# Kernel optimization log

Hardware: AMD Instinct MI355X
Metric: run time of the kernel (lower is better)

The kernel has to match this reference:

```python
import jax, jax.numpy as jnp
import numpy as np

H = 2048       # hidden_size
NH = 16        # num_attention_heads
NKV = 4        # num_key_value_heads
HD = H // NH   # head_dim = 128
INTER = 8192   # intermediate_size
L = 2048       # packed sequence length
EPS = 1e-6


def rmsnorm(x, w, eps=EPS):
    var = jnp.mean(x * x, axis=-1, keepdims=True)
    return x * jax.lax.rsqrt(var + eps) * w


def setup_inputs() -> dict:
    key = jax.random.key(0)
    ks = jax.random.split(key, 9)
    s = 0.02
    return {
        "hidden_states": jax.random.normal(ks[0], (1, L, H), jnp.float32),
        "cu_seqlens_q": jnp.array([0, 512, 1280, 2048], jnp.int32),
        "ln1_w": jnp.ones((H,), jnp.float32),
        "ln2_w": jnp.ones((H,), jnp.float32),
        "q_w": jax.random.normal(ks[1], (NH * HD, H), jnp.float32) * s,
        "k_w": jax.random.normal(ks[2], (NKV * HD, H), jnp.float32) * s,
        "v_w": jax.random.normal(ks[3], (NKV * HD, H), jnp.float32) * s,
        "o_w": jax.random.normal(ks[4], (H, NH * HD), jnp.float32) * s,
        "gate_w": jax.random.normal(ks[5], (INTER, H), jnp.float32) * s,
        "up_w": jax.random.normal(ks[6], (INTER, H), jnp.float32) * s,
        "down_w": jax.random.normal(ks[7], (H, INTER), jnp.float32) * s,
    }


def _segment_mask(cu, q_len):
    # segment id of each position: repeat_interleave of arange over lengths
    pos = jnp.arange(q_len)
    seg = jnp.searchsorted(cu[1:], pos, side="right")  # [L]
    mask = seg[:, None] == seg[None, :]
    mask = mask & (pos[None, :] <= pos[:, None])  # causal, q_len == k_len
    return mask  # [L, L] bool


def _forward(hidden_states, cu_seqlens_q, ln1_w, ln2_w, q_w, k_w, v_w, o_w,
             gate_w, up_w, down_w):
    b, q_len, _ = hidden_states.shape
    residual = hidden_states
    normed = rmsnorm(hidden_states, ln1_w)

    # project_kv
    key_states = (normed @ k_w.T).reshape(b, q_len, NKV, HD)
    value_states = (normed @ v_w.T).reshape(b, q_len, NKV, HD)

    q = (normed @ q_w.T).reshape(b, q_len, NH, HD)
    rep = NH // NKV
    k = jnp.repeat(key_states, rep, axis=2)   # repeat_interleave over heads
    v = jnp.repeat(value_states, rep, axis=2)

    scores = jnp.einsum("bqhd,bkhd->bhqk", q, k) / np.sqrt(HD)
    mask = _segment_mask(cu_seqlens_q, q_len)
    scores = jnp.where(mask[None, None, :, :], scores,
                       jnp.finfo(scores.dtype).min)
    probs = jax.nn.softmax(scores.astype(jnp.float32), axis=-1).astype(q.dtype)
    attn = jnp.einsum("bhqk,bkhd->bqhd", probs, v).reshape(b, q_len, NH * HD)
    mixed = attn @ o_w.T

    hidden = residual + mixed
    residual = hidden
    normed2 = rmsnorm(hidden, ln2_w)
    mlp = (jax.nn.silu(normed2 @ gate_w.T) * (normed2 @ up_w.T)) @ down_w.T
    hidden = residual + mlp
    return hidden, key_states, value_states


def reference(hidden_states, cu_seqlens_q, ln1_w, ln2_w, q_w, k_w, v_w, o_w,
              gate_w, up_w, down_w):
    return _forward(hidden_states, cu_seqlens_q, ln1_w, ln2_w, q_w, k_w, v_w,
                    o_w, gate_w, up_w, down_w)
```

## Files before the change

kernel.cpp:

```cpp
#include <hip/hip_runtime.h>
#include <stdint.h>

typedef __bf16 bf16;
typedef __bf16 bf16x8 __attribute__((ext_vector_type(8)));
typedef __bf16 bf16x4v __attribute__((ext_vector_type(4)));
typedef float f32x4 __attribute__((ext_vector_type(4)));

#define L_SEQ 2048
#define H_DIM 2048
#define KV_DIM 512
#define QKV_LD 3072
#define INTER_DIM 8192

__device__ __forceinline__ void load_lds16(const void* g, void* l) {
  __builtin_amdgcn_global_load_lds(
      (const __attribute__((address_space(1))) void*)g,
      (__attribute__((address_space(3))) void*)l, 16, 0, 0);
}

__global__ __launch_bounds__(256)
void cvt_all(const float* __restrict__ q, const float* __restrict__ k,
             const float* __restrict__ v, const float* __restrict__ o,
             const float* __restrict__ g, const float* __restrict__ u,
             const float* __restrict__ dn, bf16* __restrict__ WB) {
  const int b = blockIdx.x;
  const float* s;
  size_t doff;
  int lb;
  if (b < 2048)       { s = q;  doff = 0;        lb = b; }
  else if (b < 2560)  { s = k;  doff = 4194304;  lb = b - 2048; }
  else if (b < 3072)  { s = v;  doff = 5242880;  lb = b - 2560; }
  else if (b < 5120)  { s = o;  doff = 6291456;  lb = b - 3072; }
  else if (b < 13312) { s = g;  doff = 10485760; lb = b - 5120; }
  else if (b < 21504) { s = u;  doff = 27262976; lb = b - 13312; }
  else                { s = dn; doff = 44040192; lb = b - 21504; }
  const size_t i = (size_t)lb * 2048 + threadIdx.x * 8;
  float4 a = *(const float4*)(s + i);
  float4 c = *(const float4*)(s + i + 4);
  bf16x8 ov;
  ov[0] = (bf16)a.x; ov[1] = (bf16)a.y; ov[2] = (bf16)a.z; ov[3] = (bf16)a.w;
  ov[4] = (bf16)c.x; ov[5] = (bf16)c.y; ov[6] = (bf16)c.z; ov[7] = (bf16)c.w;
  *(bf16x8*)(WB + doff + i) = ov;
}

__global__ __launch_bounds__(256)
void rmsnorm_bf16(const float* __restrict__ x, const float* __restrict__ w,
                  bf16* __restrict__ out) {
  const int row = blockIdx.x;
  const int t = threadIdx.x;
  const float* xr = x + (size_t)row * H_DIM + t * 8;
  float4 a = *(const float4*)xr;
  float4 b = *(const float4*)(xr + 4);
  float ss = a.x * a.x + a.y * a.y + a.z * a.z + a.w * a.w +
             b.x * b.x + b.y * b.y + b.z * b.z + b.w * b.w;
#pragma unroll
  for (int off = 1; off < 64; off <<= 1) ss += __shfl_xor(ss, off, 64);
  __shared__ float red[4];
  if ((t & 63) == 0) red[t >> 6] = ss;
  __syncthreads();
  ss = red[0] + red[1] + red[2] + red[3];
  const float rs = rsqrtf(ss * (1.0f / H_DIM) + 1e-6f);
  float4 w1 = *(const float4*)(w + t * 8);
  float4 w2 = *(const float4*)(w + t * 8 + 4);
  bf16x8 o;
  o[0] = (bf16)(a.x * rs * w1.x);
  o[1] = (bf16)(a.y * rs * w1.y);
  o[2] = (bf16)(a.z * rs * w1.z);
  o[3] = (bf16)(a.w * rs * w1.w);
  o[4] = (bf16)(b.x * rs * w2.x);
  o[5] = (bf16)(b.y * rs * w2.y);
  o[6] = (bf16)(b.z * rs * w2.z);
  o[7] = (bf16)(b.w * rs * w2.w);
  *(bf16x8*)(out + (size_t)row * H_DIM + t * 8) = o;
}

__global__ __launch_bounds__(256)
void add_rmsnorm(const float* __restrict__ p0, const float* __restrict__ p1,
                 const float* __restrict__ res, const float* __restrict__ w,
                 float* __restrict__ hidden, bf16* __restrict__ normed) {
  const int row = blockIdx.x;
  const int t = threadIdx.x;
  const size_t base = (size_t)row * H_DIM + t * 8;
  float4 a0 = *(const float4*)(p0 + base);
  float4 a1 = *(const float4*)(p0 + base + 4);
  float4 b0 = *(const float4*)(p1 + base);
  float4 b1 = *(const float4*)(p1 + base + 4);
  float4 c0 = *(const float4*)(res + base);
  float4 c1 = *(const float4*)(res + base + 4);
  float4 h0, h1;
  h0.x = a0.x + b0.x + c0.x; h0.y = a0.y + b0.y + c0.y;
  h0.z = a0.z + b0.z + c0.z; h0.w = a0.w + b0.w + c0.w;
  h1.x = a1.x + b1.x + c1.x; h1.y = a1.y + b1.y + c1.y;
  h1.z = a1.z + b1.z + c1.z; h1.w = a1.w + b1.w + c1.w;
  *(float4*)(hidden + base) = h0;
  *(float4*)(hidden + base + 4) = h1;
  float ss = h0.x * h0.x + h0.y * h0.y + h0.z * h0.z + h0.w * h0.w +
             h1.x * h1.x + h1.y * h1.y + h1.z * h1.z + h1.w * h1.w;
#pragma unroll
  for (int off = 1; off < 64; off <<= 1) ss += __shfl_xor(ss, off, 64);
  __shared__ float red[4];
  if ((t & 63) == 0) red[t >> 6] = ss;
  __syncthreads();
  ss = red[0] + red[1] + red[2] + red[3];
  const float rs = rsqrtf(ss * (1.0f / H_DIM) + 1e-6f);
  float4 w1 = *(const float4*)(w + t * 8);
  float4 w2 = *(const float4*)(w + t * 8 + 4);
  bf16x8 o;
  o[0] = (bf16)(h0.x * rs * w1.x);
  o[1] = (bf16)(h0.y * rs * w1.y);
  o[2] = (bf16)(h0.z * rs * w1.z);
  o[3] = (bf16)(h0.w * rs * w1.w);
  o[4] = (bf16)(h1.x * rs * w2.x);
  o[5] = (bf16)(h1.y * rs * w2.y);
  o[6] = (bf16)(h1.z * rs * w2.z);
  o[7] = (bf16)(h1.w * rs * w2.w);
  *(bf16x8*)(normed + (size_t)row * H_DIM + t * 8) = o;
}

__global__ __launch_bounds__(256)
void reduce_add4(const float* __restrict__ p, size_t zs,
                 const float* __restrict__ res, float* __restrict__ out) {
  const size_t i = ((size_t)blockIdx.x * 256 + threadIdx.x) * 4;
  float4 a = *(const float4*)(p + i);
  float4 b = *(const float4*)(p + zs + i);
  float4 c = *(const float4*)(p + 2 * zs + i);
  float4 d = *(const float4*)(p + 3 * zs + i);
  float4 r = *(const float4*)(res + i);
  float4 o;
  o.x = a.x + b.x + c.x + d.x + r.x;
  o.y = a.y + b.y + c.y + d.y + r.y;
  o.z = a.z + b.z + c.z + d.z + r.z;
  o.w = a.w + b.w + c.w + d.w + r.w;
  *(float4*)(out + i) = o;
}

__global__ __launch_bounds__(256)
void qkv_combine(const float* __restrict__ p, size_t zs,
                 bf16* __restrict__ qkv, float* __restrict__ outk,
                 float* __restrict__ outv) {
  const size_t i = ((size_t)blockIdx.x * 256 + threadIdx.x) * 4;
  float4 a = *(const float4*)(p + i);
  float4 b = *(const float4*)(p + zs + i);
  float4 s;
  s.x = a.x + b.x; s.y = a.y + b.y; s.z = a.z + b.z; s.w = a.w + b.w;
  bf16x4v o;
  o[0] = (bf16)s.x; o[1] = (bf16)s.y; o[2] = (bf16)s.z; o[3] = (bf16)s.w;
  *(bf16x4v*)(qkv + i) = o;
  const int col = (int)(i % QKV_LD);
  const size_t row = i / QKV_LD;
  if (col >= 2560)      *(float4*)(outv + row * KV_DIM + (col - 2560)) = s;
  else if (col >= 2048) *(float4*)(outk + row * KV_DIM + (col - 2048)) = s;
}


#define WAIT_VM(n) asm volatile("s_waitcnt vmcnt(" #n ")" ::: "memory")

#define ISSUE_TILE(ko, base)                          \
  load_lds16(pa0 + (ko), (base) + dln);               \
  load_lds16(pa1 + (ko), (base) + 8192 + dln);        \
  load_lds16(pb0 + (ko), (base) + 16384 + dln);       \
  load_lds16(pb1 + (ko), (base) + 24576 + dln);

#define MFMA_Q(mh, nh, bfr)                                                  \
  _Pragma("unroll") for (int mi = 0; mi < 4; ++mi)                           \
      _Pragma("unroll") for (int ni = 0; ni < 2; ++ni)                       \
          acc[mh][nh][mi][ni] = __builtin_amdgcn_mfma_f32_16x16x32_bf16(     \
              af[mi], bfr[ni], acc[mh][nh][mi][ni], 0, 0, 0);

__global__ __launch_bounds__(512, 2)
void gemm32_bt(const bf16* __restrict__ A, int lda,
               const bf16* __restrict__ B, int ldb, int kpb,
               float* __restrict__ outf, int ldof, size_t zstride) {
  __shared__ __align__(16) char smb[98304];
  const int t = threadIdx.x;
  const int lane = t & 63;
  const int l15 = lane & 15, l4 = lane >> 4;
  const int wid = t >> 6;
  const int wr = wid >> 2, wc = wid & 3;

  const int gn = gridDim.x;
  const int bid = blockIdx.y * gn + blockIdx.x;
  int mb, nb;
  if ((gn & 7) == 0) {
    const int j = bid & 7, local = bid >> 3, npx = gn >> 3;
    nb = j * npx + local % npx;
    mb = local / npx;
  } else {
    nb = bid % gn;
    mb = bid / gn;
  }
  const int m0 = mb * 256, n0 = nb * 256;
  const int kbeg = blockIdx.z * kpb;
  const int NT = kpb >> 5;

  int aoff[4], boff[2];
#pragma unroll
  for (int mi = 0; mi < 4; ++mi) {
    const int rA = wr * 64 + mi * 16 + l15;
    aoff[mi] = rA * 64 + ((l4 ^ ((rA >> 1) & 3)) << 4);
  }
#pragma unroll
  for (int ni = 0; ni < 2; ++ni) {
    const int rB = wc * 32 + ni * 16 + l15;
    boff[ni] = rB * 64 + ((l4 ^ ((rB >> 1) & 3)) << 4);
  }

  const int r = t >> 2;
  const int gsw = (((t & 3) ^ ((r >> 1) & 3)) << 3);
  const bf16* pa0 = A + (size_t)(m0 + r) * lda + kbeg + gsw;
  const bf16* pa1 = A + (size_t)(m0 + 128 + r) * lda + kbeg + gsw;
  const bf16* pb0 = B + (size_t)(n0 + r) * ldb + kbeg + gsw;
  const bf16* pb1 = B + (size_t)(n0 + 128 + r) * ldb + kbeg + gsw;
  const int dln = t * 16;

  ISSUE_TILE(0, smb);
  if (NT > 1) { ISSUE_TILE(32, smb + 32768); }

  const f32x4 zero = {0.f, 0.f, 0.f, 0.f};
  f32x4 acc[2][2][4][2];
#pragma unroll
  for (int mh = 0; mh < 2; ++mh)
#pragma unroll
    for (int nh = 0; nh < 2; ++nh)
#pragma unroll
      for (int mi = 0; mi < 4; ++mi)
#pragma unroll
        for (int ni = 0; ni < 2; ++ni) acc[mh][nh][mi][ni] = zero;

  int br = 0, bw = 2;
#pragma unroll 1
  for (int tt = 0; tt < NT; ++tt) {
    if (tt + 1 < NT) { WAIT_VM(4); } else { WAIT_VM(0); }
    __builtin_amdgcn_s_barrier();
    if (tt + 2 < NT) {
      char* dst = smb + bw * 32768;
      const int ko = (tt + 2) * 32;
      ISSUE_TILE(ko, dst);
    }
    const char* bb = smb + br * 32768;
    const char* cA0 = bb;
    const char* cA1 = bb + 8192;
    const char* cB0 = bb + 16384;
    const char* cB1 = bb + 24576;

    bf16x8 af[4], b0f[2], b1f[2];
#pragma unroll
    for (int mi = 0; mi < 4; ++mi)
      af[mi] = *(const bf16x8*)(cA0 + aoff[mi]);
#pragma unroll
    for (int ni = 0; ni < 2; ++ni) b0f[ni] = *(const bf16x8*)(cB0 + boff[ni]);
#pragma unroll
    for (int ni = 0; ni < 2; ++ni) b1f[ni] = *(const bf16x8*)(cB1 + boff[ni]);
    MFMA_Q(0, 0, b0f);
    MFMA_Q(0, 1, b1f);
#pragma unroll
    for (int mi = 0; mi < 4; ++mi)
      af[mi] = *(const bf16x8*)(cA1 + aoff[mi]);
    MFMA_Q(1, 0, b0f);
    MFMA_Q(1, 1, b1f);

    br = (br == 2) ? 0 : br + 1;
    bw = (bw == 2) ? 0 : bw + 1;
  }

  float* outz = outf + zstride * blockIdx.z;
#pragma unroll
  for (int mh = 0; mh < 2; ++mh)
#pragma unroll
    for (int nh = 0; nh < 2; ++nh)
#pragma unroll
      for (int mi = 0; mi < 4; ++mi)
#pragma unroll
        for (int ni = 0; ni < 2; ++ni) {
          const int row0 = m0 + mh * 128 + wr * 64 + mi * 16 + l4 * 4;
          const int col = n0 + nh * 128 + wc * 32 + ni * 16 + l15;
#pragma unroll
          for (int rr2 = 0; rr2 < 4; ++rr2)
            outz[(size_t)(row0 + rr2) * ldof + col] = acc[mh][nh][mi][ni][rr2];
        }
}

__global__ __launch_bounds__(512, 2)
void gemm32_glu(const bf16* __restrict__ A, const bf16* __restrict__ Bg,
                const bf16* __restrict__ Bu, bf16* __restrict__ out) {
  __shared__ __align__(16) char smb[98304];
  const int t = threadIdx.x;
  const int lane = t & 63;
  const int l15 = lane & 15, l4 = lane >> 4;
  const int wid = t >> 6;
  const int wr = wid >> 2, wc = wid & 3;

  const int gn = gridDim.x;
  const int bid = blockIdx.y * gn + blockIdx.x;
  const int j = bid & 7, local = bid >> 3, npx = gn >> 3;
  const int nb = j * npx + local % npx;
  const int mb = local / npx;
  const int m0 = mb * 256, n0 = nb * 128;
  const int NT = H_DIM / 32;

  int aoff[4], boff[2];
#pragma unroll
  for (int mi = 0; mi < 4; ++mi) {
    const int rA = wr * 64 + mi * 16 + l15;
    aoff[mi] = rA * 64 + ((l4 ^ ((rA >> 1) & 3)) << 4);
  }
#pragma unroll
  for (int ni = 0; ni < 2; ++ni) {
    const int rB = wc * 32 + ni * 16 + l15;
    boff[ni] = rB * 64 + ((l4 ^ ((rB >> 1) & 3)) << 4);
  }

  const int r = t >> 2;
  const int gsw = (((t & 3) ^ ((r >> 1) & 3)) << 3);
  const bf16* pa0 = A + (size_t)(m0 + r) * H_DIM + gsw;
  const bf16* pa1 = A + (size_t)(m0 + 128 + r) * H_DIM + gsw;
  const bf16* pb0 = Bg + (size_t)(n0 + r) * H_DIM + gsw;
  const bf16* pb1 = Bu + (size_t)(n0 + r) * H_DIM + gsw;
  const int dln = t * 16;

  ISSUE_TILE(0, smb);
  ISSUE_TILE(32, smb + 32768);

  const f32x4 zero = {0.f, 0.f, 0.f, 0.f};
  f32x4 acc[2][2][4][2];
#pragma unroll
  for (int mh = 0; mh < 2; ++mh)
#pragma unroll
    for (int nh = 0; nh < 2; ++nh)
#pragma unroll
      for (int mi = 0; mi < 4; ++mi)
#pragma unroll
        for (int ni = 0; ni < 2; ++ni) acc[mh][nh][mi][ni] = zero;

  int br = 0, bw = 2;
#pragma unroll 1
  for (int tt = 0; tt < NT; ++tt) {
    if (tt + 1 < NT) { WAIT_VM(4); } else { WAIT_VM(0); }
    __builtin_amdgcn_s_barrier();
    if (tt + 2 < NT) {
      char* dst = smb + bw * 32768;
      const int ko = (tt + 2) * 32;
      ISSUE_TILE(ko, dst);
    }
    const char* bb = smb + br * 32768;
    const char* cA0 = bb;
    const char* cA1 = bb + 8192;
    const char* cB0 = bb + 16384;
    const char* cB1 = bb + 24576;

    bf16x8 af[4], b0f[2], b1f[2];
#pragma unroll
    for (int mi = 0; mi < 4; ++mi)
      af[mi] = *(const bf16x8*)(cA0 + aoff[mi]);
#pragma unroll
    for (int ni = 0; ni < 2; ++ni) b0f[ni] = *(const bf16x8*)(cB0 + boff[ni]);
#pragma unroll
    for (int ni = 0; ni < 2; ++ni) b1f[ni] = *(const bf16x8*)(cB1 + boff[ni]);
    MFMA_Q(0, 0, b0f);
    MFMA_Q(0, 1, b1f);
#pragma unroll
    for (int mi = 0; mi < 4; ++mi)
      af[mi] = *(const bf16x8*)(cA1 + aoff[mi]);
    MFMA_Q(1, 0, b0f);
    MFMA_Q(1, 1, b1f);

    br = (br == 2) ? 0 : br + 1;
    bw = (bw == 2) ? 0 : bw + 1;
  }

#pragma unroll
  for (int mh = 0; mh < 2; ++mh)
#pragma unroll
    for (int mi = 0; mi < 4; ++mi)
#pragma unroll
      for (int ni = 0; ni < 2; ++ni) {
        const int row0 = m0 + mh * 128 + wr * 64 + mi * 16 + l4 * 4;
        const int col = n0 + wc * 32 + ni * 16 + l15;
#pragma unroll
        for (int rr2 = 0; rr2 < 4; ++rr2) {
          const float g = acc[mh][0][mi][ni][rr2];
          const float u = acc[mh][1][mi][ni][rr2];
          const float sg = g / (1.f + __expf(-g));
          out[(size_t)(row0 + rr2) * INTER_DIM + col] = (bf16)(sg * u);
        }
      }
}

__global__ __launch_bounds__(256, 3)
void gemm_bt(const bf16* __restrict__ A, int lda,
             const bf16* __restrict__ B, int ldb, int kpb,
             float* __restrict__ outf, int ldof, size_t zstride) {
  __shared__ bf16 sA[2 * 128 * 32];
  __shared__ bf16 sB[2 * 128 * 32];
  const int t = threadIdx.x;
  const int lane = t & 63;
  const int l15 = lane & 15, l4 = lane >> 4;
  const int wm = ((t >> 6) >> 1) * 64;
  const int wn = ((t >> 6) & 1) * 64;
  const int m0 = blockIdx.y * 128;
  const int n0 = blockIdx.x * 128;
  const int kbeg = blockIdx.z * kpb;
  const int kend = kbeg + kpb;

  const f32x4 zero = {0.f, 0.f, 0.f, 0.f};
  f32x4 acc[4][4];
#pragma unroll
  for (int i = 0; i < 4; ++i)
#pragma unroll
    for (int j = 0; j < 4; ++j) acc[i][j] = zero;

  for (int k0 = kbeg; k0 < kend; k0 += 64) {
#pragma unroll
    for (int i = 0; i < 4; ++i) {
      const int flat = i * 4096 + t * 16;
      const int kc = flat >> 13;
      const int wb = flat & 8191;
      const int r = wb >> 6, ce = (wb & 63) >> 1;
      const int gc = k0 + kc * 32 + ce;
      load_lds16(A + (size_t)(m0 + r) * lda + gc, (char*)sA + flat);
      load_lds16(B + (size_t)(n0 + r) * ldb + gc, (char*)sB + flat);
    }
    __syncthreads();

#pragma unroll
    for (int kc = 0; kc < 2; ++kc) {
      bf16x8 af[4], bfr[4];
#pragma unroll
      for (int mi = 0; mi < 4; ++mi)
        af[mi] = *(const bf16x8*)(&sA[kc * 4096 + (wm + mi * 16 + l15) * 32 +
                                      l4 * 8]);
#pragma unroll
      for (int ni = 0; ni < 4; ++ni)
        bfr[ni] = *(const bf16x8*)(&sB[kc * 4096 + (wn + ni * 16 + l15) * 32 +
                                       l4 * 8]);
#pragma unroll
      for (int mi = 0; mi < 4; ++mi)
#pragma unroll
        for (int ni = 0; ni < 4; ++ni)
          acc[mi][ni] = __builtin_amdgcn_mfma_f32_16x16x32_bf16(
              af[mi], bfr[ni], acc[mi][ni], 0, 0, 0);
    }
    __syncthreads();
  }

#pragma unroll
  for (int mi = 0; mi < 4; ++mi) {
#pragma unroll
    for (int ni = 0; ni < 4; ++ni) {
      const int row0 = m0 + wm + mi * 16 + l4 * 4;
      const int col = n0 + wn + ni * 16 + l15;
#pragma unroll
      for (int r = 0; r < 4; ++r)
        outf[zstride * blockIdx.z + (size_t)(row0 + r) * ldof + col] =
            acc[mi][ni][r];
    }
  }
}

__global__ __launch_bounds__(256, 2)
void attn_fwd(const bf16* __restrict__ qkv, const int* __restrict__ cu,
              bf16* __restrict__ out) {
  const int h = blockIdx.y;
  const int q0 = blockIdx.x * 64;
  const int kvh = h >> 2;
  const int t = threadIdx.x;
  const int lane = t & 63;
  const int w = t >> 6;
  const int l15 = lane & 15, l4 = lane >> 4;

  __shared__ bf16 sK[64 * 136];
  __shared__ bf16 sVt[128 * 72];
  __shared__ bf16 sP[4][16 * 64];

  const int c1 = cu[1], c2 = cu[2];
  const int seg0 = (q0 >= c2) ? c2 : ((q0 >= c1) ? c1 : 0);

  const int qrow = q0 + w * 16 + l15;
  bf16x8 qf[4];
#pragma unroll
  for (int kc = 0; kc < 4; ++kc) {
    bf16x8 v = *(const bf16x8*)(qkv + (size_t)qrow * QKV_LD + h * 128 +
                                kc * 32 + l4 * 8);
#pragma unroll
    for (int j = 0; j < 8; ++j)
      v[j] = (bf16)((float)v[j] * 0.08838834764831845f);
    qf[kc] = v;
  }

  const f32x4 zero = {0.f, 0.f, 0.f, 0.f};
  f32x4 oacc[8];
#pragma unroll
  for (int i = 0; i < 8; ++i) oacc[i] = zero;
  float mi[4] = {-1e30f, -1e30f, -1e30f, -1e30f};
  float li[4] = {0.f, 0.f, 0.f, 0.f};

  for (int k0 = seg0; k0 <= q0; k0 += 64) {
#pragma unroll
    for (int it = 0; it < 4; ++it) {
      const int flat = it * 4096 + t * 16;
      const int r = flat >> 8, db = flat & 255;
      *(bf16x8*)((char*)sK + r * 272 + db) = *(const bf16x8*)(
          (const char*)(qkv + (size_t)(k0 + r) * QKV_LD + 2048 + kvh * 128) +
          db);
      const int chunk = it * 256 + t;
      const int vr = chunk & 63, dc = chunk >> 6;
      bf16x8 vv = *(const bf16x8*)(qkv + (size_t)(k0 + vr) * QKV_LD + 2560 +
                                   kvh * 128 + dc * 8);
#pragma unroll
      for (int j = 0; j < 8; ++j) sVt[(dc * 8 + j) * 72 + vr] = vv[j];
    }
    __syncthreads();

    f32x4 sacc[4];
#pragma unroll
    for (int kg = 0; kg < 4; ++kg) {
      f32x4 a = zero;
#pragma unroll
      for (int kc = 0; kc < 4; ++kc) {
        bf16x8 kf = *(const bf16x8*)((const char*)sK + (kg * 16 + l15) * 272 +
                                     kc * 64 + l4 * 16);
        a = __builtin_amdgcn_mfma_f32_16x16x32_bf16(qf[kc], kf, a, 0, 0, 0);
      }
      sacc[kg] = a;
    }

    if (k0 == q0) {
#pragma unroll
      for (int kg = 0; kg < 4; ++kg) {
        const int kk = kg * 16 + l15;
#pragma unroll
        for (int r = 0; r < 4; ++r) {
          const int qq = w * 16 + l4 * 4 + r;
          if (kk > qq) sacc[kg][r] = -1e30f;
        }
      }
    }

    float mx[4], al[4], rs[4];
#pragma unroll
    for (int r = 0; r < 4; ++r)
      mx[r] = fmaxf(fmaxf(sacc[0][r], sacc[1][r]),
                    fmaxf(sacc[2][r], sacc[3][r]));
#pragma unroll
    for (int off = 1; off < 16; off <<= 1)
#pragma unroll
      for (int r = 0; r < 4; ++r)
        mx[r] = fmaxf(mx[r], __shfl_xor(mx[r], off, 64));
#pragma unroll
    for (int r = 0; r < 4; ++r) {
      const float mn = fmaxf(mi[r], mx[r]);
      al[r] = __expf(mi[r] - mn);
      mi[r] = mn;
      rs[r] = 0.f;
    }
#pragma unroll
    for (int kg = 0; kg < 4; ++kg)
#pragma unroll
      for (int r = 0; r < 4; ++r) {
        const float p = __expf(sacc[kg][r] - mi[r]);
        sacc[kg][r] = p;
        rs[r] += p;
      }
#pragma unroll
    for (int off = 1; off < 16; off <<= 1)
#pragma unroll
      for (int r = 0; r < 4; ++r) rs[r] += __shfl_xor(rs[r], off, 64);
#pragma unroll
    for (int r = 0; r < 4; ++r) li[r] = li[r] * al[r] + rs[r];
#pragma unroll
    for (int dn = 0; dn < 8; ++dn)
#pragma unroll
      for (int r = 0; r < 4; ++r) oacc[dn][r] *= al[r];

#pragma unroll
    for (int kg = 0; kg < 4; ++kg)
#pragma unroll
      for (int r = 0; r < 4; ++r)
        sP[w][(l4 * 4 + r) * 64 + kg * 16 + l15] = (bf16)sacc[kg][r];

    bf16x8 pf[2];
#pragma unroll
    for (int kc2 = 0; kc2 < 2; ++kc2)
      pf[kc2] = *(const bf16x8*)(&sP[w][l15 * 64 + kc2 * 32 + l4 * 8]);
#pragma unroll
    for (int dn = 0; dn < 8; ++dn)
#pragma unroll
      for (int kc2 = 0; kc2 < 2; ++kc2) {
        bf16x8 vf = *(const bf16x8*)(&sVt[(dn * 16 + l15) * 72 + kc2 * 32 +
                                          l4 * 8]);
        oacc[dn] = __builtin_amdgcn_mfma_f32_16x16x32_bf16(pf[kc2], vf,
                                                           oacc[dn], 0, 0, 0);
      }
    __syncthreads();
  }

#pragma unroll
  for (int dn = 0; dn < 8; ++dn)
#pragma unroll
    for (int r = 0; r < 4; ++r) {
      const size_t m = (size_t)(q0 + w * 16 + l4 * 4 + r);
      out[m * H_DIM + h * 128 + dn * 16 + l15] = (bf16)(oacc[dn][r] / li[r]);
    }
}

extern "C" void kernel_launch(void* const* d_in, const int* in_sizes, int n_in,
                              void* d_out, int out_size, void* d_ws,
                              size_t ws_size, hipStream_t stream) {
  (void)in_sizes; (void)n_in; (void)out_size; (void)ws_size;
  const float* hs     = (const float*)d_in[0];
  const int*   cu     = (const int*)d_in[1];
  const float* ln1    = (const float*)d_in[2];
  const float* ln2    = (const float*)d_in[3];
  const float* q_w    = (const float*)d_in[4];
  const float* k_w    = (const float*)d_in[5];
  const float* v_w    = (const float*)d_in[6];
  const float* o_w    = (const float*)d_in[7];
  const float* gate_w = (const float*)d_in[8];
  const float* up_w   = (const float*)d_in[9];
  const float* down_w = (const float*)d_in[10];

  float* out_hidden = (float*)d_out;
  float* out_k = out_hidden + (size_t)L_SEQ * H_DIM;
  float* out_v = out_k + (size_t)L_SEQ * KV_DIM;

  char* ws = (char*)d_ws;
  bf16* WB = (bf16*)ws;
  const size_t wq_off = 0;
  const size_t wo_off = 6291456;
  const size_t wg_off = 10485760;
  const size_t wu_off = 27262976;
  const size_t wd_off = 44040192;

  bf16*  normed1 = (bf16*)(ws + ((size_t)116 << 20));
  bf16*  qkv     = (bf16*)(ws + ((size_t)124 << 20));
  bf16*  attnb   = (bf16*)(ws + ((size_t)136 << 20));
  bf16*  normed2 = (bf16*)(ws + ((size_t)144 << 20));
  bf16*  interb  = (bf16*)(ws + ((size_t)152 << 20));
  float* qpart   = (float*)(ws + ((size_t)136 << 20));
  float* opart   = (float*)(ws + ((size_t)152 << 20));
  float* dpart   = (float*)(ws);

  dim3 blk(256);

  cvt_all<<<29696, blk, 0, stream>>>(q_w, k_w, v_w, o_w, gate_w, up_w, down_w,
                                     WB);

  rmsnorm_bf16<<<L_SEQ, blk, 0, stream>>>(hs, ln1, normed1);

  gemm32_bt<<<dim3(12, 8, 2), dim3(512), 0, stream>>>(
      normed1, H_DIM, WB + wq_off, H_DIM, 1024, qpart, QKV_LD,
      (size_t)L_SEQ * QKV_LD);
  qkv_combine<<<6144, blk, 0, stream>>>(qpart, (size_t)L_SEQ * QKV_LD, qkv,
                                        out_k, out_v);

  attn_fwd<<<dim3(32, 16), blk, 0, stream>>>(qkv, cu, attnb);

  gemm_bt<<<dim3(16, 16, 2), blk, 0, stream>>>(
      attnb, H_DIM, WB + wo_off, H_DIM, 1024, opart, H_DIM,
      (size_t)L_SEQ * H_DIM);

  add_rmsnorm<<<L_SEQ, blk, 0, stream>>>(opart, opart + (size_t)L_SEQ * H_DIM,
                                         hs, ln2, out_hidden, normed2);

  gemm32_glu<<<dim3(64, 8), dim3(512), 0, stream>>>(normed2, WB + wg_off,
                                                    WB + wu_off, interb);

  gemm32_bt<<<dim3(8, 8, 4), dim3(512), 0, stream>>>(
      interb, INTER_DIM, WB + wd_off, INTER_DIM, 2048, dpart, H_DIM,
      (size_t)L_SEQ * H_DIM);

  reduce_add4<<<4096, blk, 0, stream>>>(dpart, (size_t)L_SEQ * H_DIM,
                                        out_hidden, out_hidden);
}
```

Before: 594.6 us.

## Interleave LDS fragment loads and global prefetch with MFMA quarters in GEMM k-loop

Moves the GEMM k-loop into a shared engine that splits each k-tile into four MFMA quarters. Each quarter is interleaved with one global-to-LDS prefetch and the LDS fragment reads for the next quarter or tile, with sched_barrier fences and setprio around the MFMA groups. Fragments for the next tile are preloaded before the loop ends, so LDS latency hides behind matrix math instead of stalling before it. The cost is a second barrier per tile and more live fragment registers, which could hurt occupancy at 2 blocks per CU.

```diff
diff --git a/kernel.cpp b/kernel.cpp
--- a/kernel.cpp
+++ b/kernel.cpp
@@ -153,19 +153,106 @@
 }
 
 
-#define WAIT_VM(n) asm volatile("s_waitcnt vmcnt(" #n ")" ::: "memory")
-
-#define ISSUE_TILE(ko, base)                          \
-  load_lds16(pa0 + (ko), (base) + dln);               \
-  load_lds16(pa1 + (ko), (base) + 8192 + dln);        \
-  load_lds16(pb0 + (ko), (base) + 16384 + dln);       \
-  load_lds16(pb1 + (ko), (base) + 24576 + dln);
-
-#define MFMA_Q(mh, nh, bfr)                                                  \
-  _Pragma("unroll") for (int mi = 0; mi < 4; ++mi)                           \
-      _Pragma("unroll") for (int ni = 0; ni < 2; ++ni)                       \
-          acc[mh][nh][mi][ni] = __builtin_amdgcn_mfma_f32_16x16x32_bf16(     \
-              af[mi], bfr[ni], acc[mh][nh][mi][ni], 0, 0, 0);
+#define WAIT_VM_N(n) asm volatile("s_waitcnt vmcnt(" #n ")" ::: "memory")
+#define SBAR() __builtin_amdgcn_sched_barrier(0)
+
+#define MFMA8(mh, nh, afv, bfv)                                            \
+  _Pragma("unroll") for (int mi = 0; mi < 4; ++mi)                         \
+      _Pragma("unroll") for (int ni = 0; ni < 2; ++ni)                     \
+          acc[mh][nh][mi][ni] = __builtin_amdgcn_mfma_f32_16x16x32_bf16(   \
+              afv[mi], bfv[ni], acc[mh][nh][mi][ni], 0, 0, 0);
+
+__device__ __forceinline__ void kloop_engine(
+    const bf16* __restrict__ pa0, const bf16* __restrict__ pa1,
+    const bf16* __restrict__ pb0, const bf16* __restrict__ pb1,
+    char* smb, int dln, const int aoff[4], const int boff[2], int NT,
+    f32x4 (&acc)[2][2][4][2]) {
+  load_lds16(pa0, smb + dln);
+  load_lds16(pb0, smb + 16384 + dln);
+  load_lds16(pb1, smb + 24576 + dln);
+  load_lds16(pa1, smb + 8192 + dln);
+  load_lds16(pa0 + 32, smb + 32768 + dln);
+  load_lds16(pb0 + 32, smb + 32768 + 16384 + dln);
+  load_lds16(pb1 + 32, smb + 32768 + 24576 + dln);
+  load_lds16(pa1 + 32, smb + 32768 + 8192 + dln);
+  WAIT_VM_N(6);
+  __builtin_amdgcn_s_barrier();
+
+  bf16x8 afC[4], afN[4], b0f[2], b1f[2];
+#pragma unroll
+  for (int mi = 0; mi < 4; ++mi) afC[mi] = *(const bf16x8*)(smb + aoff[mi]);
+#pragma unroll
+  for (int ni = 0; ni < 2; ++ni)
+    b0f[ni] = *(const bf16x8*)(smb + 16384 + boff[ni]);
+
+  int br = 0, bw = 2;
+#pragma unroll 1
+  for (int tt = 0; tt < NT; ++tt) {
+    const char* bb = smb + br * 32768;
+    const int bn = (br == 2) ? 0 : br + 1;
+    const char* nb = smb + bn * 32768;
+    char* dst = smb + bw * 32768;
+    const int ko = (tt + 2) * 32;
+    const bool st1 = (tt + 1 < NT), st2 = (tt + 2 < NT);
+
+    if (st1) { WAIT_VM_N(4); } else { WAIT_VM_N(0); }
+    __builtin_amdgcn_s_barrier();
+    SBAR();
+
+    if (st2) load_lds16(pa0 + ko, dst + dln);
+#pragma unroll
+    for (int ni = 0; ni < 2; ++ni)
+      b1f[ni] = *(const bf16x8*)(bb + 24576 + boff[ni]);
+    SBAR();
+    __builtin_amdgcn_s_setprio(1);
+    MFMA8(0, 0, afC, b0f);
+    __builtin_amdgcn_s_setprio(0);
+    SBAR();
+
+    if (st2) load_lds16(pb0 + ko, dst + 16384 + dln);
+#pragma unroll
+    for (int mi = 0; mi < 4; ++mi)
+      afN[mi] = *(const bf16x8*)(bb + 8192 + aoff[mi]);
+    SBAR();
+    __builtin_amdgcn_s_setprio(1);
+    MFMA8(0, 1, afC, b1f);
+    __builtin_amdgcn_s_setprio(0);
+    SBAR();
+
+    if (st1) {
+      if (st2) { WAIT_VM_N(4); } else { WAIT_VM_N(2); }
+      __builtin_amdgcn_s_barrier();
+      SBAR();
+    }
+
+    if (st2) load_lds16(pb1 + ko, dst + 24576 + dln);
+    if (st1) {
+#pragma unroll
+      for (int mi = 0; mi < 4; ++mi)
+        afC[mi] = *(const bf16x8*)(nb + aoff[mi]);
+    }
+    SBAR();
+    __builtin_amdgcn_s_setprio(1);
+    MFMA8(1, 0, afN, b0f);
+    __builtin_amdgcn_s_setprio(0);
+    SBAR();
+
+    if (st2) load_lds16(pa1 + ko, dst + 8192 + dln);
+    if (st1) {
+#pragma unroll
+      for (int ni = 0; ni < 2; ++ni)
+        b0f[ni] = *(const bf16x8*)(nb + 16384 + boff[ni]);
+    }
+    SBAR();
+    __builtin_amdgcn_s_setprio(1);
+    MFMA8(1, 1, afN, b1f);
+    __builtin_amdgcn_s_setprio(0);
+    SBAR();
+
+    br = bn;
+    bw = (bw == 2) ? 0 : bw + 1;
+  }
+}
 
 __global__ __launch_bounds__(512, 2)
 void gemm32_bt(const bf16* __restrict__ A, int lda,
@@ -213,9 +300,6 @@
   const bf16* pb1 = B + (size_t)(n0 + 128 + r) * ldb + kbeg + gsw;
   const int dln = t * 16;
 
-  ISSUE_TILE(0, smb);
-  if (NT > 1) { ISSUE_TILE(32, smb + 32768); }
-
   const f32x4 zero = {0.f, 0.f, 0.f, 0.f};
   f32x4 acc[2][2][4][2];
 #pragma unroll
@@ -227,41 +311,7 @@
 #pragma unroll
         for (int ni = 0; ni < 2; ++ni) acc[mh][nh][mi][ni] = zero;
 
-  int br = 0, bw = 2;
-#pragma unroll 1
-  for (int tt = 0; tt < NT; ++tt) {
-    if (tt + 1 < NT) { WAIT_VM(4); } else { WAIT_VM(0); }
-    __builtin_amdgcn_s_barrier();
-    if (tt + 2 < NT) {
-      char* dst = smb + bw * 32768;
-      const int ko = (tt + 2) * 32;
-      ISSUE_TILE(ko, dst);
-    }
-    const char* bb = smb + br * 32768;
-    const char* cA0 = bb;
-    const char* cA1 = bb + 8192;
-    const char* cB0 = bb + 16384;
-    const char* cB1 = bb + 24576;
-
-    bf16x8 af[4], b0f[2], b1f[2];
-#pragma unroll
-    for (int mi = 0; mi < 4; ++mi)
-      af[mi] = *(const bf16x8*)(cA0 + aoff[mi]);
-#pragma unroll
-    for (int ni = 0; ni < 2; ++ni) b0f[ni] = *(const bf16x8*)(cB0 + boff[ni]);
-#pragma unroll
-    for (int ni = 0; ni < 2; ++ni) b1f[ni] = *(const bf16x8*)(cB1 + boff[ni]);
-    MFMA_Q(0, 0, b0f);
-    MFMA_Q(0, 1, b1f);
-#pragma unroll
-    for (int mi = 0; mi < 4; ++mi)
-      af[mi] = *(const bf16x8*)(cA1 + aoff[mi]);
-    MFMA_Q(1, 0, b0f);
-    MFMA_Q(1, 1, b1f);
-
-    br = (br == 2) ? 0 : br + 1;
-    bw = (bw == 2) ? 0 : bw + 1;
-  }
+  kloop_engine(pa0, pa1, pb0, pb1, smb, dln, aoff, boff, NT, acc);
 
   float* outz = outf + zstride * blockIdx.z;
 #pragma unroll
@@ -318,9 +368,6 @@
   const bf16* pb1 = Bu + (size_t)(n0 + r) * H_DIM + gsw;
   const int dln = t * 16;
 
-  ISSUE_TILE(0, smb);
-  ISSUE_TILE(32, smb + 32768);
-
   const f32x4 zero = {0.f, 0.f, 0.f, 0.f};
   f32x4 acc[2][2][4][2];
 #pragma unroll
@@ -332,41 +379,7 @@
 #pragma unroll
         for (int ni = 0; ni < 2; ++ni) acc[mh][nh][mi][ni] = zero;
 
-  int br = 0, bw = 2;
-#pragma unroll 1
-  for (int tt = 0; tt < NT; ++tt) {
-    if (tt + 1 < NT) { WAIT_VM(4); } else { WAIT_VM(0); }
-    __builtin_amdgcn_s_barrier();
-    if (tt + 2 < NT) {
-      char* dst = smb + bw * 32768;
-      const int ko = (tt + 2) * 32;
-      ISSUE_TILE(ko, dst);
-    }
-    const char* bb = smb + br * 32768;
-    const char* cA0 = bb;
-    const char* cA1 = bb + 8192;
-    const char* cB0 = bb + 16384;
-    const char* cB1 = bb + 24576;
-
-    bf16x8 af[4], b0f[2], b1f[2];
-#pragma unroll
-    for (int mi = 0; mi < 4; ++mi)
-      af[mi] = *(const bf16x8*)(cA0 + aoff[mi]);
-#pragma unroll
-    for (int ni = 0; ni < 2; ++ni) b0f[ni] = *(const bf16x8*)(cB0 + boff[ni]);
-#pragma unroll
-    for (int ni = 0; ni < 2; ++ni) b1f[ni] = *(const bf16x8*)(cB1 + boff[ni]);
-    MFMA_Q(0, 0, b0f);
-    MFMA_Q(0, 1, b1f);
-#pragma unroll
-    for (int mi = 0; mi < 4; ++mi)
-      af[mi] = *(const bf16x8*)(cA1 + aoff[mi]);
-    MFMA_Q(1, 0, b0f);
-    MFMA_Q(1, 1, b1f);
-
-    br = (br == 2) ? 0 : br + 1;
-    bw = (bw == 2) ? 0 : bw + 1;
-  }
+  kloop_engine(pa0, pa1, pb0, pb1, smb, dln, aoff, boff, NT, acc);
 
 #pragma unroll
   for (int mh = 0; mh < 2; ++mh)
```

Measured after the change: 601.7 us. About the same (+1.2%).
